# Performance work log

Hardware: AMD Instinct MI355X
Metric: run time of the kernel (lower is better)

The kernel has to match this reference:

```python
import jax, jax.numpy as jnp
import numpy as np

B, T, C = 4, 2048, 1024
N_HEAD = 16
HEAD = C // N_HEAD

def setup_inputs() -> dict:
    key = jax.random.key(0)
    ks = jax.random.split(key, 5)
    return {
        "x": jax.random.normal(ks[0], (B, T, C), dtype=jnp.float32),
        "W_attn": jax.random.normal(ks[1], (C, 3 * C), dtype=jnp.float32) * (C ** -0.5),
        "b_attn": jax.random.normal(ks[2], (3 * C,), dtype=jnp.float32) * 0.02,
        "W_proj": jax.random.normal(ks[3], (C, C), dtype=jnp.float32) * (C ** -0.5),
        "b_proj": jax.random.normal(ks[4], (C,), dtype=jnp.float32) * 0.02,
    }

def reference(x, W_attn, b_attn, W_proj, b_proj):
    Bx, Tx, Cx = x.shape
    qkv = x @ W_attn + b_attn  # [B,T,3C]
    q, k, v = jnp.split(qkv, 3, axis=2)
    # [B,T,H,D] -> [B,H,T,D]
    q = q.reshape(Bx, Tx, N_HEAD, HEAD).transpose(0, 2, 1, 3)
    k = k.reshape(Bx, Tx, N_HEAD, HEAD).transpose(0, 2, 1, 3)
    v = v.reshape(Bx, Tx, N_HEAD, HEAD).transpose(0, 2, 1, 3)
    att = jnp.einsum('bhqd,bhkd->bhqk', q, k) * (HEAD ** -0.5)
    causal = jnp.tril(jnp.ones((Tx, Tx), dtype=bool))
    att = jnp.where(causal, att, jnp.float32(-jnp.inf))
    att = jax.nn.softmax(att, axis=-1)
    y = jnp.einsum('bhqk,bhkd->bhqd', att, v)
    y = y.transpose(0, 2, 1, 3).reshape(Bx, Tx, Cx)
    return y @ W_proj + b_proj
```

## Files before the change

kernel.cpp:

```cpp
#include <hip/hip_runtime.h>
#include <stdint.h>

#define NB 4
#define TT 2048
#define CC 1024
#define NH 16
#define DD 64
#define BHH (NB*NH)
#define MROWS (NB*TT)

typedef uint16_t u16;
typedef uint32_t u32;
typedef __bf16 bf16x8 __attribute__((ext_vector_type(8)));
typedef float f32x4 __attribute__((ext_vector_type(4)));
typedef float f32x16 __attribute__((ext_vector_type(16)));

__device__ __forceinline__ u16 f2bf(float f) {
    union { float f; uint32_t u; } v; v.f = f;
    uint32_t u = v.u;
    return (u16)((u + 0x7FFF + ((u >> 16) & 1)) >> 16);
}

__device__ __forceinline__ u32 cvtpk(float lo, float hi) {
    u32 r;
    asm volatile("v_cvt_pk_bf16_f32 %0, %1, %2" : "=v"(r) : "v"(lo), "v"(hi));
    return r;
}

__device__ __forceinline__ void plswap(u32& a, u32& b) {
    asm volatile("v_permlane32_swap_b32 %0, %1" : "+v"(a), "+v"(b));
}

__device__ __forceinline__ bf16x8 mk8(u32 a, u32 b, u32 c, u32 d) {
    union { u32 u[4]; bf16x8 v; } x;
    x.u[0] = a; x.u[1] = b; x.u[2] = c; x.u[3] = d;
    return x.v;
}

__device__ __forceinline__ void gl_lds16(const u16* g, u16* l) {
    __builtin_amdgcn_global_load_lds(
        (const __attribute__((address_space(1))) unsigned int*)g,
        (__attribute__((address_space(3))) unsigned int*)l, 16, 0, 0);
}

__device__ __forceinline__ f32x4 mfma16(bf16x8 a, bf16x8 b, f32x4 c) {
    return __builtin_amdgcn_mfma_f32_16x16x32_bf16(a, b, c, 0, 0, 0);
}
__device__ __forceinline__ f32x16 mfma32(bf16x8 a, bf16x8 b, f32x16 c) {
    return __builtin_amdgcn_mfma_f32_32x32x16_bf16(a, b, c, 0, 0, 0);
}

__global__ __launch_bounds__(256) void k_f2b(const float* __restrict__ in,
                                             u16* __restrict__ out, int n) {
    const int i = (blockIdx.x * 256 + threadIdx.x) * 4;
    if (i >= n) return;
    const float4 v = *(const float4*)(in + i);
    ushort4 o;
    o.x = f2bf(v.x); o.y = f2bf(v.y); o.z = f2bf(v.z); o.w = f2bf(v.w);
    *(ushort4*)(out + i) = o;
}

__global__ __launch_bounds__(256) void k_transpose_cvt(const float* __restrict__ in,
                                                       u16* __restrict__ out,
                                                       int R, int N) {
    __shared__ float t[32][33];
    const int n0 = blockIdx.x * 32, r0 = blockIdx.y * 32;
    const int c  = threadIdx.x & 31, rq = threadIdx.x >> 5;
#pragma unroll
    for (int i = 0; i < 4; ++i) {
        int r = rq + i * 8;
        t[r][c] = in[(r0 + r) * N + n0 + c];
    }
    __syncthreads();
#pragma unroll
    for (int i = 0; i < 4; ++i) {
        int r = rq + i * 8;
        out[(n0 + r) * R + r0 + c] = f2bf(t[c][r]);
    }
}

__device__ __forceinline__ void gemm128v2(const u16* __restrict__ A,
                                          const u16* __restrict__ Bt,
                                          int m0, int n0, f32x4 acc[4][4]) {
    __shared__ __align__(16) u16 As[2][128 * 64];
    __shared__ __align__(16) u16 Bs[2][128 * 64];
    const int tid = threadIdx.x, l = tid & 63, w = tid >> 6;
    const int wr = w >> 1, wc = w & 1;
    const int lr = l & 15, lg = l >> 4;

    auto stage = [&](int kt, int b) {
#pragma unroll
        for (int line = 0; line < 4; ++line) {
            const int s = line * 4096 + tid * 16;
            const int row = s >> 7;
            const int colb = (s & 127) ^ ((row & 7) << 4);
            const int ldsoff = (line * 4096 + w * 1024) >> 1;
            gl_lds16(A  + (size_t)(m0 + row) * 1024 + kt * 64 + (colb >> 1),
                     &As[b][ldsoff]);
            gl_lds16(Bt + (size_t)(n0 + row) * 1024 + kt * 64 + (colb >> 1),
                     &Bs[b][ldsoff]);
        }
    };

    stage(0, 0);
    __syncthreads();

    for (int kt = 0; kt < 16; ++kt) {
        const int b = kt & 1;
        if (kt < 15) stage(kt + 1, b ^ 1);
#pragma unroll
        for (int ks = 0; ks < 2; ++ks) {
            bf16x8 af[4], bf[4];
#pragma unroll
            for (int m = 0; m < 4; ++m) {
                const int row = wr * 64 + m * 16 + lr;
                const int byteC = (ks * 64 + lg * 16) ^ ((row & 7) << 4);
                af[m] = *(const bf16x8*)&As[b][(row * 128 + byteC) >> 1];
            }
#pragma unroll
            for (int n = 0; n < 4; ++n) {
                const int row = wc * 64 + n * 16 + lr;
                const int byteC = (ks * 64 + lg * 16) ^ ((row & 7) << 4);
                bf[n] = *(const bf16x8*)&Bs[b][(row * 128 + byteC) >> 1];
            }
#pragma unroll
            for (int m = 0; m < 4; ++m)
#pragma unroll
                for (int n = 0; n < 4; ++n)
                    acc[m][n] = mfma16(af[m], bf[n], acc[m][n]);
        }
        __syncthreads();
    }
}

__global__ __launch_bounds__(256, 2) void k_gemm_qkv(const u16* __restrict__ X,
                                                     const u16* __restrict__ Wt,
                                                     const float* __restrict__ bias,
                                                     u16* __restrict__ Qo,
                                                     u16* __restrict__ Ko,
                                                     u16* __restrict__ Vto) {
    const int id = blockIdx.x;
    const int xcd = id & 7, lid = id >> 3;
    const int lm = lid & 7, ln = lid >> 3;
    const int m0 = (xcd * 8 + lm) * 128;
    const int n0 = ln * 128;

    f32x4 acc[4][4];
#pragma unroll
    for (int m = 0; m < 4; ++m)
#pragma unroll
        for (int n = 0; n < 4; ++n) acc[m][n] = (f32x4){0.f, 0.f, 0.f, 0.f};
    gemm128v2(X, Wt, m0, n0, acc);

    const float C2 = 0.18033688011112042f;
    const int tid = threadIdx.x, l = tid & 63, w = tid >> 6;
    const int wr = w >> 1, wc = w & 1, lr = l & 15, lg = l >> 4;
#pragma unroll
    for (int n = 0; n < 4; ++n) {
        const int c = n0 + wc * 64 + n * 16 + lr;
        const float bv = bias[c];
        const int which = c >> 10, cc = c & 1023, h = cc >> 6, d = cc & 63;
#pragma unroll
        for (int m = 0; m < 4; ++m) {
            const int rbase = m0 + wr * 64 + m * 16 + lg * 4;
#pragma unroll
            for (int j = 0; j < 4; ++j) {
                const int r = rbase + j;
                const int b = r >> 11, t = r & 2047;
                const int bh = b * NH + h;
                const float v = acc[m][n][j] + bv;
                if (which == 0)      Qo[(bh * TT + t) * DD + d] = f2bf(v * C2);
                else if (which == 1) Ko[(bh * TT + t) * DD + d] = f2bf(v);
                else                 Vto[(bh * DD + d) * TT + t] = f2bf(v);
            }
        }
    }
}

__global__ __launch_bounds__(256, 2) void k_gemm_proj(const u16* __restrict__ Yin,
                                                      const u16* __restrict__ Wt,
                                                      const float* __restrict__ bias,
                                                      float* __restrict__ out) {
    const int id = blockIdx.x;
    const int xcd = id & 7, lid = id >> 3;
    const int lm = lid & 7, ln = lid >> 3;
    const int m0 = (xcd * 8 + lm) * 128;
    const int n0 = ln * 128;

    f32x4 acc[4][4];
#pragma unroll
    for (int m = 0; m < 4; ++m)
#pragma unroll
        for (int n = 0; n < 4; ++n) acc[m][n] = (f32x4){0.f, 0.f, 0.f, 0.f};
    gemm128v2(Yin, Wt, m0, n0, acc);

    const int tid = threadIdx.x, l = tid & 63, w = tid >> 6;
    const int wr = w >> 1, wc = w & 1, lr = l & 15, lg = l >> 4;
#pragma unroll
    for (int n = 0; n < 4; ++n) {
        const int c = n0 + wc * 64 + n * 16 + lr;
        const float bv = bias[c];
#pragma unroll
        for (int m = 0; m < 4; ++m) {
            const int rbase = m0 + wr * 64 + m * 16 + lg * 4;
#pragma unroll
            for (int j = 0; j < 4; ++j) {
                const int r = rbase + j;
                out[r * CC + c] = acc[m][n][j] + bv;
            }
        }
    }
}

__global__ __launch_bounds__(256) void k_attn(const u16* __restrict__ Qg_,
                                              const u16* __restrict__ Kg_,
                                              const u16* __restrict__ Vg_,
                                              u16* __restrict__ Y) {
    __shared__ __align__(16) u16 Ks[2][64 * 64];
    __shared__ __align__(16) u16 Vs[2][64 * 64];

    const int id = blockIdx.x;
    const int g = id >> 6;
    const int qperm[16] = {15,14,13,12, 0,1,2,3, 11,10,9,8, 4,5,6,7};
    const int qi = qperm[g];
    const int bh = id & 63;
    const int q0 = qi * 128;
    const u16* Qg = Qg_ + (size_t)bh * TT * DD;
    const u16* Kg = Kg_ + (size_t)bh * TT * DD;
    const u16* Vg = Vg_ + (size_t)bh * DD * TT;
    const int tid = threadIdx.x, l = tid & 63, w = tid >> 6;
    const int lq = l & 31, hi = l >> 5;
    const int qs = q0 + w * 32;

    unsigned dmask = 0;
#pragma unroll
    for (int r = 0; r < 16; ++r) {
        const int kvloc = (r & 3) + 8 * (r >> 2) + 4 * hi;
        if (kvloc > lq) dmask |= (1u << r);
    }

    const u16* qrow = Qg + (qs + lq) * DD + hi * 8;
    bf16x8 qf0 = *(const bf16x8*)(qrow);
    bf16x8 qf1 = *(const bf16x8*)(qrow + 16);
    bf16x8 qf2 = *(const bf16x8*)(qrow + 32);
    bf16x8 qf3 = *(const bf16x8*)(qrow + 48);

    const bf16x8 onesf = mk8(0x3F803F80u, 0x3F803F80u, 0x3F803F80u, 0x3F803F80u);

    f32x16 o0 = {}, o1 = {}, lsum = {};
    float mrun = -1e30f;
    const int nt = 2 * qi + 2;

    auto stage = [&](int t, int b) {
        const int kv0 = t * 64;
#pragma unroll
        for (int iss = 0; iss < 2; ++iss) {
            const int s = iss * 4096 + tid * 16;
            const int row = s >> 7;
            const int colb = (s & 127) ^ ((row & 7) << 4);
            const int ldsoff = (iss * 4096 + w * 1024) >> 1;
            gl_lds16(Kg + (kv0 + row) * DD + (colb >> 1), &Ks[b][ldsoff]);
            gl_lds16(Vg + row * TT + kv0 + (colb >> 1),   &Vs[b][ldsoff]);
        }
    };

    stage(0, 0);
    __syncthreads();

    for (int t = 0; t < nt; ++t) {
        const int b = t & 1;
        if (t + 1 < nt) stage(t + 1, b ^ 1);
        const int kv0 = t * 64;

#pragma unroll
        for (int s = 0; s < 2; ++s) {
            const int kvs = kv0 + 32 * s;
            if (kvs > qs) continue;

            f32x16 st = {};
#pragma unroll
            for (int i = 0; i < 4; ++i) {
                const int row = 32 * s + lq;
                const int byte = (32 * i + 16 * hi) ^ ((row & 7) << 4);
                const bf16x8 kf = *(const bf16x8*)&Ks[b][(row * 128 + byte) >> 1];
                if (i == 0) st = mfma32(kf, qf0, st);
                else if (i == 1) st = mfma32(kf, qf1, st);
                else if (i == 2) st = mfma32(kf, qf2, st);
                else st = mfma32(kf, qf3, st);
            }

            if (kvs == qs) {
#pragma unroll
                for (int r = 0; r < 16; ++r)
                    if ((dmask >> r) & 1) st[r] = -1e30f;
            }

            float mx = st[0];
#pragma unroll
            for (int r = 1; r < 16; ++r) mx = fmaxf(mx, st[r]);
            mx = fmaxf(mx, __shfl_xor(mx, 32));

            if (!__all(mx <= mrun)) {
                const float mn = fmaxf(mrun, mx);
                const float scl = __builtin_amdgcn_exp2f(mrun - mn);
                mrun = mn;
                lsum[0] *= scl;
#pragma unroll
                for (int r = 0; r < 16; ++r) { o0[r] *= scl; o1[r] *= scl; }
            }

            u32 pk0, pk1, pk2, pk3, pk4, pk5, pk6, pk7;
            {
                float pa, pb;
                pa = __builtin_amdgcn_exp2f(st[0] - mrun);
                pb = __builtin_amdgcn_exp2f(st[1] - mrun);
                pk0 = cvtpk(pa, pb);
                pa = __builtin_amdgcn_exp2f(st[2] - mrun);
                pb = __builtin_amdgcn_exp2f(st[3] - mrun);
                pk1 = cvtpk(pa, pb);
                pa = __builtin_amdgcn_exp2f(st[4] - mrun);
                pb = __builtin_amdgcn_exp2f(st[5] - mrun);
                pk2 = cvtpk(pa, pb);
                pa = __builtin_amdgcn_exp2f(st[6] - mrun);
                pb = __builtin_amdgcn_exp2f(st[7] - mrun);
                pk3 = cvtpk(pa, pb);
                pa = __builtin_amdgcn_exp2f(st[8] - mrun);
                pb = __builtin_amdgcn_exp2f(st[9] - mrun);
                pk4 = cvtpk(pa, pb);
                pa = __builtin_amdgcn_exp2f(st[10] - mrun);
                pb = __builtin_amdgcn_exp2f(st[11] - mrun);
                pk5 = cvtpk(pa, pb);
                pa = __builtin_amdgcn_exp2f(st[12] - mrun);
                pb = __builtin_amdgcn_exp2f(st[13] - mrun);
                pk6 = cvtpk(pa, pb);
                pa = __builtin_amdgcn_exp2f(st[14] - mrun);
                pb = __builtin_amdgcn_exp2f(st[15] - mrun);
                pk7 = cvtpk(pa, pb);
            }

            plswap(pk0, pk2); plswap(pk1, pk3);
            plswap(pk4, pk6); plswap(pk5, pk7);
            const bf16x8 pf0 = mk8(pk0, pk1, pk2, pk3);
            const bf16x8 pf1 = mk8(pk4, pk5, pk6, pk7);

            lsum = mfma32(onesf, pf0, lsum);
            lsum = mfma32(onesf, pf1, lsum);

#pragma unroll
            for (int dh = 0; dh < 2; ++dh) {
#pragma unroll
                for (int ks = 0; ks < 2; ++ks) {
                    const int row = 32 * dh + lq;
                    const int byte = (64 * s + 32 * ks + 16 * hi) ^ ((row & 7) << 4);
                    const bf16x8 vf = *(const bf16x8*)&Vs[b][(row * 128 + byte) >> 1];
                    if (dh == 0) o0 = mfma32(vf, ks ? pf1 : pf0, o0);
                    else         o1 = mfma32(vf, ks ? pf1 : pf0, o1);
                }
            }
        }
        if (t + 1 < nt) __syncthreads();
    }

    const float inv = 1.0f / lsum[0];
    const int bb = bh >> 4, h = bh & 15;
    u16* yrow = Y + (size_t)(bb * TT + qs + lq) * CC + h * DD;
#pragma unroll
    for (int rq = 0; rq < 4; ++rq) {
        const int d0 = 8 * rq + 4 * hi;
        const u32 w0 = cvtpk(o0[rq * 4 + 0] * inv, o0[rq * 4 + 1] * inv);
        const u32 w1 = cvtpk(o0[rq * 4 + 2] * inv, o0[rq * 4 + 3] * inv);
        *(uint2*)&yrow[d0] = make_uint2(w0, w1);
        const u32 w2 = cvtpk(o1[rq * 4 + 0] * inv, o1[rq * 4 + 1] * inv);
        const u32 w3 = cvtpk(o1[rq * 4 + 2] * inv, o1[rq * 4 + 3] * inv);
        *(uint2*)&yrow[32 + d0] = make_uint2(w2, w3);
    }
}

extern "C" void kernel_launch(void* const* d_in, const int* in_sizes, int n_in,
                              void* d_out, int out_size, void* d_ws, size_t ws_size,
                              hipStream_t stream) {
    const float* X  = (const float*)d_in[0];
    const float* Wa = (const float*)d_in[1];
    const float* ba = (const float*)d_in[2];
    const float* Wp = (const float*)d_in[3];
    const float* bp = (const float*)d_in[4];
    float* out = (float*)d_out;

    u16* ws  = (u16*)d_ws;
    u16* Xb  = ws;
    u16* WtA = Xb + (size_t)MROWS * CC;
    u16* WtP = WtA + 3072 * 1024;
    u16* Qb  = WtP + 1024 * 1024;
    u16* Kb  = Qb + (size_t)BHH * TT * DD;
    u16* Vtb = Kb + (size_t)BHH * TT * DD;
    u16* Yb  = Vtb + (size_t)BHH * TT * DD;

    k_f2b<<<dim3(MROWS * CC / 1024), 256, 0, stream>>>(X, Xb, MROWS * CC);
    k_transpose_cvt<<<dim3(96, 32), 256, 0, stream>>>(Wa, WtA, 1024, 3072);
    k_transpose_cvt<<<dim3(32, 32), 256, 0, stream>>>(Wp, WtP, 1024, 1024);
    k_gemm_qkv<<<dim3(1536), 256, 0, stream>>>(Xb, WtA, ba, Qb, Kb, Vtb);
    k_attn<<<dim3(1024), 256, 0, stream>>>(Qb, Kb, Vtb, Yb);
    k_gemm_proj<<<dim3(512), 256, 0, stream>>>(Yb, WtP, bp, out);
}
```

Before: 209.6 us.

## Use lazy max rescaling, scalar row-sum, and simple descending query order in attention

The online-softmax max update now fires only when the new tile max exceeds the running max by more than 8 (in log2 units), so the O rescale is skipped on most tiles. The row sum is kept in a per-lane float and combined with one shuffle at the end, which removes two MFMA instructions per tile that previously computed it with a ones-vector multiply. The block-to-query-tile permutation is replaced by a plain descending order. Lazy rescaling lets exponentials reach up to 2^8, which slightly reduces bf16 precision headroom, and the new block order changes how work is balanced across CUs.

```diff
diff --git a/kernel.cpp b/kernel.cpp
--- a/kernel.cpp
+++ b/kernel.cpp
@@ -220,9 +220,7 @@
     __shared__ __align__(16) u16 Vs[2][64 * 64];
 
     const int id = blockIdx.x;
-    const int g = id >> 6;
-    const int qperm[16] = {15,14,13,12, 0,1,2,3, 11,10,9,8, 4,5,6,7};
-    const int qi = qperm[g];
+    const int qi = 15 - (id >> 6);
     const int bh = id & 63;
     const int q0 = qi * 128;
     const u16* Qg = Qg_ + (size_t)bh * TT * DD;
@@ -245,10 +243,8 @@
     bf16x8 qf2 = *(const bf16x8*)(qrow + 32);
     bf16x8 qf3 = *(const bf16x8*)(qrow + 48);
 
-    const bf16x8 onesf = mk8(0x3F803F80u, 0x3F803F80u, 0x3F803F80u, 0x3F803F80u);
-
-    f32x16 o0 = {}, o1 = {}, lsum = {};
-    float mrun = -1e30f;
+    f32x16 o0 = {}, o1 = {};
+    float mrun = -1e30f, lrun = 0.f;
     const int nt = 2 * qi + 2;
 
     auto stage = [&](int t, int b) {
@@ -300,51 +296,50 @@
             for (int r = 1; r < 16; ++r) mx = fmaxf(mx, st[r]);
             mx = fmaxf(mx, __shfl_xor(mx, 32));
 
-            if (!__all(mx <= mrun)) {
+            if (!__all(mx - mrun <= 8.0f)) {
                 const float mn = fmaxf(mrun, mx);
                 const float scl = __builtin_amdgcn_exp2f(mrun - mn);
                 mrun = mn;
-                lsum[0] *= scl;
+                lrun *= scl;
 #pragma unroll
                 for (int r = 0; r < 16; ++r) { o0[r] *= scl; o1[r] *= scl; }
             }
 
+            float psum = 0.f;
             u32 pk0, pk1, pk2, pk3, pk4, pk5, pk6, pk7;
             {
                 float pa, pb;
                 pa = __builtin_amdgcn_exp2f(st[0] - mrun);
                 pb = __builtin_amdgcn_exp2f(st[1] - mrun);
-                pk0 = cvtpk(pa, pb);
+                psum += pa + pb; pk0 = cvtpk(pa, pb);
                 pa = __builtin_amdgcn_exp2f(st[2] - mrun);
                 pb = __builtin_amdgcn_exp2f(st[3] - mrun);
-                pk1 = cvtpk(pa, pb);
+                psum += pa + pb; pk1 = cvtpk(pa, pb);
                 pa = __builtin_amdgcn_exp2f(st[4] - mrun);
                 pb = __builtin_amdgcn_exp2f(st[5] - mrun);
-                pk2 = cvtpk(pa, pb);
+                psum += pa + pb; pk2 = cvtpk(pa, pb);
                 pa = __builtin_amdgcn_exp2f(st[6] - mrun);
                 pb = __builtin_amdgcn_exp2f(st[7] - mrun);
-                pk3 = cvtpk(pa, pb);
+                psum += pa + pb; pk3 = cvtpk(pa, pb);
                 pa = __builtin_amdgcn_exp2f(st[8] - mrun);
                 pb = __builtin_amdgcn_exp2f(st[9] - mrun);
-                pk4 = cvtpk(pa, pb);
+                psum += pa + pb; pk4 = cvtpk(pa, pb);
                 pa = __builtin_amdgcn_exp2f(st[10] - mrun);
                 pb = __builtin_amdgcn_exp2f(st[11] - mrun);
-                pk5 = cvtpk(pa, pb);
+                psum += pa + pb; pk5 = cvtpk(pa, pb);
                 pa = __builtin_amdgcn_exp2f(st[12] - mrun);
                 pb = __builtin_amdgcn_exp2f(st[13] - mrun);
-                pk6 = cvtpk(pa, pb);
+                psum += pa + pb; pk6 = cvtpk(pa, pb);
                 pa = __builtin_amdgcn_exp2f(st[14] - mrun);
                 pb = __builtin_amdgcn_exp2f(st[15] - mrun);
-                pk7 = cvtpk(pa, pb);
-            }
+                psum += pa + pb; pk7 = cvtpk(pa, pb);
+            }
+            lrun += psum;
 
             plswap(pk0, pk2); plswap(pk1, pk3);
             plswap(pk4, pk6); plswap(pk5, pk7);
             const bf16x8 pf0 = mk8(pk0, pk1, pk2, pk3);
             const bf16x8 pf1 = mk8(pk4, pk5, pk6, pk7);
-
-            lsum = mfma32(onesf, pf0, lsum);
-            lsum = mfma32(onesf, pf1, lsum);
 
 #pragma unroll
             for (int dh = 0; dh < 2; ++dh) {
@@ -361,7 +356,8 @@
         if (t + 1 < nt) __syncthreads();
     }
 
-    const float inv = 1.0f / lsum[0];
+    lrun += __shfl_xor(lrun, 32);
+    const float inv = 1.0f / lrun;
     const int bb = bh >> 4, h = bh & 15;
     u16* yrow = Y + (size_t)(bb * TT + qs + lq) * CC + h * DD;
 #pragma unroll
```

Result: faster. 177.2 us (-15.4%).
